# Kernel tuning notes

Measured on AMD Instinct MI355X. Metric: run time of the kernel, lower is better.

Reference implementation:

```python
import jax, jax.numpy as jnp
import numpy as np


def setup_inputs() -> dict:
    key = jax.random.key(0)
    k1, k2 = jax.random.split(key)
    x_in = jax.random.normal(k1, (8, 16384, 64), dtype=jnp.float32)
    codebook = jax.random.normal(k2, (512, 64), dtype=jnp.float32)
    return {"x_in": x_in, "codebook": codebook}


def reference(x_in, codebook):
    # Euclidean distances x_in [B,N,D] vs codebook [K,D] -> [B,N,K]
    x_sq = jnp.sum(x_in * x_in, axis=-1, keepdims=True)            # [B,N,1]
    e_sq = jnp.sum(codebook * codebook, axis=-1)                   # [K]
    cross = jnp.einsum('bnd,kd->bnk', x_in, codebook)              # [B,N,K]
    d2 = x_sq + e_sq[None, None, :] - 2.0 * cross
    distances = jnp.sqrt(jnp.maximum(d2, 0.0))
    # argmin with keepdim, as in extract_indices
    indices = jnp.argmin(distances, axis=2, keepdims=True)         # [B,N,1]
    # apply_codebook: embedding lookup -> [B,N,1,D]
    quantized = codebook[indices]
    return quantized
```

## Files before the change

### kernel.cpp

```cpp
#include <hip/hip_runtime.h>

#define D    64
#define K    512
#define QTOT (8 * 16384)
#define THR  0.001f

typedef __attribute__((ext_vector_type(8))) short short8;
typedef __attribute__((ext_vector_type(4))) short short4v;
typedef __attribute__((ext_vector_type(4))) float f32x4;

__device__ __forceinline__ unsigned short f2bf(float f) {
    unsigned u = __builtin_bit_cast(unsigned, f);
    u = u + 0x7FFFu + ((u >> 16) & 1u);
    return (unsigned short)(u >> 16);
}
__device__ __forceinline__ float bf2f(unsigned short h) {
    unsigned u = ((unsigned)h) << 16;
    return __builtin_bit_cast(float, u);
}

__global__ __launch_bounds__(512) void prep2b_kernel(const float* __restrict__ cb,
        float* __restrict__ esq, unsigned short* __restrict__ eh2,
        unsigned short* __restrict__ el2) {
    const int tid = threadIdx.x;
    const int b   = blockIdx.x;
    const float4* cbv4 = (const float4*)cb;
    for (int c = b * 512 + tid; c < (K * D) / 4; c += 4096) {
        float4 v = cbv4[c];
        float vv[4] = {v.x, v.y, v.z, v.w};
        short4v hi, lo;
        #pragma unroll
        for (int j = 0; j < 4; ++j) {
            unsigned short hb = f2bf(vv[j]);
            float hf = bf2f(hb);
            unsigned short lb = f2bf(vv[j] - hf);
            hi[j] = (short)f2bf(-2.0f * hf);
            lo[j] = (short)f2bf(-2.0f * bf2f(lb));
        }
        ((short4v*)eh2)[c] = hi;
        ((short4v*)el2)[c] = lo;
    }
    if (tid < 64) {
        const int row = b * 64 + tid;
        const float4* rp = (const float4*)(cb + (size_t)row * D);
        float s = 0.f;
        #pragma unroll
        for (int i = 0; i < 16; ++i) {
            float4 v = rp[i];
            s = fmaf(v.x, v.x, s); s = fmaf(v.y, v.y, s);
            s = fmaf(v.z, v.z, s); s = fmaf(v.w, v.w, s);
        }
        esq[row] = s;
    }
}

__global__ __launch_bounds__(1024) void vq_mfma12(
        const float* __restrict__ x, const float* __restrict__ cb,
        const float* __restrict__ g_esq, const unsigned short* __restrict__ eh2,
        const unsigned short* __restrict__ el2, float* __restrict__ out) {

    __shared__ unsigned short s_e[2][K * D];
    __shared__ float s_esq[K];

    const int tid  = threadIdx.x;
    const int lane = tid & 63;
    const int qrow = lane & 15;
    const int kg   = lane >> 4;
    const int kg4  = kg * 4;
    const int wv   = __builtin_amdgcn_readfirstlane(tid >> 6);
    const int qw   = blockIdx.x * 512 + wv * 32;

    for (int c = tid; c < (K * D) / 8; c += 1024) {
        short8 hv = ((const short8*)eh2)[c];
        short8 lv = ((const short8*)el2)[c];
        int byteoff = c * 16;
        int row     = byteoff >> 7;
        int addr    = byteoff ^ ((row & 7) << 4);
        *(short8*)((char*)s_e[0] + addr) = hv;
        *(short8*)((char*)s_e[1] + addr) = lv;
    }
    if (tid < K) s_esq[tid] = g_esq[tid];
    __syncthreads();

    short8 xh[2][2], xl[2][2];
    #pragma unroll
    for (int qt = 0; qt < 2; ++qt) {
        #pragma unroll
        for (int h = 0; h < 2; ++h) {
            const float* p = x + (size_t)(qw + qt * 16 + qrow) * D + h * 32 + kg * 8;
            float4 v0 = *(const float4*)p;
            float4 v1 = *(const float4*)(p + 4);
            float vv[8] = {v0.x, v0.y, v0.z, v0.w, v1.x, v1.y, v1.z, v1.w};
            short8 th, tl;
            #pragma unroll
            for (int j = 0; j < 8; ++j) {
                unsigned short hb = f2bf(vv[j]);
                th[j] = (short)hb;
                tl[j] = (short)f2bf(vv[j] - bf2f(hb));
            }
            xh[qt][h] = th;
            xl[qt][h] = tl;
        }
    }

    float m1[2], m2[2];
    int   i1[2];
    #pragma unroll
    for (int qt = 0; qt < 2; ++qt) { m1[qt] = 3.4e38f; m2[qt] = 3.4e38f; i1[qt] = 0; }

    const int swz = (qrow & 7) << 4;
    const int ob  = qrow * 128 + kg * 16;
    const char* ph = (const char*)s_e[0];
    const char* pl = (const char*)s_e[1];
    const int o0 = ob ^ swz;
    const int o1 = (ob + 64) ^ swz;
    const float* pq = s_esq + kg4;

    #pragma unroll
    for (int t = 0; t < 32; ++t) {
        short8 eh0 = *(const short8*)(ph + o0 + t * 2048);
        short8 eh1 = *(const short8*)(ph + o1 + t * 2048);
        short8 el0 = *(const short8*)(pl + o0 + t * 2048);
        short8 el1 = *(const short8*)(pl + o1 + t * 2048);
        f32x4 eqv  = *(const f32x4*)(pq + t * 16);

        __builtin_amdgcn_s_setprio(1);
        f32x4 a0 = eqv, a1 = eqv;
        a0 = __builtin_amdgcn_mfma_f32_16x16x32_bf16(eh0, xh[0][0], a0, 0, 0, 0);
        a1 = __builtin_amdgcn_mfma_f32_16x16x32_bf16(eh0, xh[1][0], a1, 0, 0, 0);
        a0 = __builtin_amdgcn_mfma_f32_16x16x32_bf16(eh1, xh[0][1], a0, 0, 0, 0);
        a1 = __builtin_amdgcn_mfma_f32_16x16x32_bf16(eh1, xh[1][1], a1, 0, 0, 0);
        a0 = __builtin_amdgcn_mfma_f32_16x16x32_bf16(eh0, xl[0][0], a0, 0, 0, 0);
        a1 = __builtin_amdgcn_mfma_f32_16x16x32_bf16(eh0, xl[1][0], a1, 0, 0, 0);
        a0 = __builtin_amdgcn_mfma_f32_16x16x32_bf16(eh1, xl[0][1], a0, 0, 0, 0);
        a1 = __builtin_amdgcn_mfma_f32_16x16x32_bf16(eh1, xl[1][1], a1, 0, 0, 0);
        a0 = __builtin_amdgcn_mfma_f32_16x16x32_bf16(el0, xh[0][0], a0, 0, 0, 0);
        a1 = __builtin_amdgcn_mfma_f32_16x16x32_bf16(el0, xh[1][0], a1, 0, 0, 0);
        a0 = __builtin_amdgcn_mfma_f32_16x16x32_bf16(el1, xh[0][1], a0, 0, 0, 0);
        a1 = __builtin_amdgcn_mfma_f32_16x16x32_bf16(el1, xh[1][1], a1, 0, 0, 0);
        __builtin_amdgcn_s_setprio(0);

        #pragma unroll
        for (int r = 0; r < 4; ++r) {
            float dd = a0[r];
            int   kc = (t * 16) | (kg4 + r);
            bool  lt = dd < m1[0];
            m2[0] = fminf(fmaxf(m1[0], dd), m2[0]);
            m1[0] = lt ? dd : m1[0];
            i1[0] = lt ? kc : i1[0];
        }
        #pragma unroll
        for (int r = 0; r < 4; ++r) {
            float dd = a1[r];
            int   kc = (t * 16) | (kg4 + r);
            bool  lt = dd < m1[1];
            m2[1] = fminf(fmaxf(m1[1], dd), m2[1]);
            m1[1] = lt ? dd : m1[1];
            i1[1] = lt ? kc : i1[1];
        }
    }

    #pragma unroll
    for (int qt = 0; qt < 2; ++qt) {
        #pragma unroll
        for (int off = 16; off <= 32; off <<= 1) {
            float om1 = __shfl_xor(m1[qt], off, 64);
            float om2 = __shfl_xor(m2[qt], off, 64);
            int   oi  = __shfl_xor(i1[qt], off, 64);
            bool  lt  = om1 < m1[qt];
            float loser = lt ? m1[qt] : om1;
            m2[qt] = fminf(fminf(m2[qt], om2), loser);
            m1[qt] = lt ? om1 : m1[qt];
            i1[qt] = lt ? oi  : i1[qt];
        }
    }

    #pragma unroll
    for (int qt = 0; qt < 2; ++qt) {
        bool flag = (m2[qt] - m1[qt]) <= THR;
        unsigned long long mask = __ballot(flag && (lane < 16));
        while (mask) {
            int ql = __ffsll(mask) - 1;
            mask &= mask - 1;
            int qf = qw + qt * 16 + ql;
            const float* xq = x + (size_t)qf * D;
            float bb = 3.4e38f;
            int   bq = 0;
            #pragma unroll 1
            for (int c0 = 0; c0 < 8; ++c0) {
                int kc = lane * 8 + c0;
                const float4* ep = (const float4*)(cb + (size_t)kc * D);
                float a = 0.f;
                #pragma unroll
                for (int i = 0; i < 16; ++i) {
                    float4 e = ep[i];
                    a = fmaf(xq[4 * i + 0], e.x, a);
                    a = fmaf(xq[4 * i + 1], e.y, a);
                    a = fmaf(xq[4 * i + 2], e.z, a);
                    a = fmaf(xq[4 * i + 3], e.w, a);
                }
                float dd = fmaf(-2.f, a, s_esq[kc]);
                if (dd < bb) { bb = dd; bq = kc; }
            }
            #pragma unroll
            for (int off = 1; off < 64; off <<= 1) {
                float ob = __shfl_xor(bb, off, 64);
                int   oq = __shfl_xor(bq, off, 64);
                if (ob < bb || (ob == bb && oq < bq)) { bb = ob; bq = oq; }
            }
            if (qrow == ql) i1[qt] = bq;
        }
    }

    #pragma unroll
    for (int qt = 0; qt < 2; ++qt) {
        size_t q = (size_t)(qw + qt * 16 + qrow);
        const float4* src = (const float4*)(cb + (size_t)i1[qt] * D) + kg * 4;
        float4*       dst = (float4*)(out + q * D) + kg * 4;
        #pragma unroll
        for (int s = 0; s < 4; ++s) dst[s] = src[s];
    }
}

__global__ __launch_bounds__(512) void vq_mfma(
        const float* __restrict__ x, const float* __restrict__ cb,
        float* __restrict__ out) {

    __shared__ unsigned short s_e[2][K * D];
    __shared__ float s_esq[K];

    const int tid  = threadIdx.x;
    const int lane = tid & 63;
    const int qrow = lane & 15;
    const int kg   = lane >> 4;
    const int wv   = __builtin_amdgcn_readfirstlane(tid >> 6);
    const int qw   = blockIdx.x * 512 + wv * 64;

    const float4* cbv4 = (const float4*)cb;
    for (int c = tid; c < (K * D) / 4; c += 512) {
        float4 v = cbv4[c];
        float vv[4] = {v.x, v.y, v.z, v.w};
        short4v hi, lo;
        #pragma unroll
        for (int j = 0; j < 4; ++j) {
            unsigned short hb = f2bf(vv[j]);
            hi[j] = (short)hb;
            lo[j] = (short)f2bf(vv[j] - bf2f(hb));
        }
        int byteoff = c * 8;
        int row     = byteoff >> 7;
        int addr    = byteoff ^ ((row & 7) << 4);
        *(short4v*)((char*)s_e[0] + addr) = hi;
        *(short4v*)((char*)s_e[1] + addr) = lo;
    }
    {
        float s = 0.f;
        #pragma unroll
        for (int d = 0; d < D; ++d) {
            float v = cb[tid * D + d];
            s = fmaf(v, v, s);
        }
        s_esq[tid] = s;
    }
    __syncthreads();

    short8 xh[4][2], xl[4][2];
    #pragma unroll
    for (int qt = 0; qt < 4; ++qt) {
        #pragma unroll
        for (int h = 0; h < 2; ++h) {
            const float* p = x + (size_t)(qw + qt * 16 + qrow) * D + h * 32 + kg * 8;
            float4 v0 = *(const float4*)p;
            float4 v1 = *(const float4*)(p + 4);
            float vv[8] = {v0.x, v0.y, v0.z, v0.w, v1.x, v1.y, v1.z, v1.w};
            short8 th, tl;
            #pragma unroll
            for (int j = 0; j < 8; ++j) {
                unsigned short hb = f2bf(vv[j]);
                th[j] = (short)hb;
                tl[j] = (short)f2bf(vv[j] - bf2f(hb));
            }
            xh[qt][h] = th;
            xl[qt][h] = tl;
        }
    }

    float m1[4], m2[4];
    int   i1[4];
    #pragma unroll
    for (int qt = 0; qt < 4; ++qt) { m1[qt] = 3.4e38f; m2[qt] = 3.4e38f; i1[qt] = 0; }

    const f32x4 zacc = {0.f, 0.f, 0.f, 0.f};

    for (int t = 0; t < 32; ++t) {
        const int row  = t * 16 + qrow;
        const int swz  = (row & 7) << 4;
        const int off0 = row * 128 + kg * 16;
        short8 eh0 = *(const short8*)((const char*)s_e[0] + ((off0     ) ^ swz));
        short8 eh1 = *(const short8*)((const char*)s_e[0] + ((off0 + 64) ^ swz));
        short8 el0 = *(const short8*)((const char*)s_e[1] + ((off0     ) ^ swz));
        short8 el1 = *(const short8*)((const char*)s_e[1] + ((off0 + 64) ^ swz));
        f32x4 eq = *(const f32x4*)(s_esq + t * 16 + kg * 4);

        #pragma unroll
        for (int qt = 0; qt < 4; ++qt) {
            f32x4 acc;
            asm volatile(
                "s_nop 3\n\t"
                "v_mfma_f32_16x16x32_bf16 %0, %1, %5, %9\n\t"
                "v_mfma_f32_16x16x32_bf16 %0, %2, %6, %0\n\t"
                "v_mfma_f32_16x16x32_bf16 %0, %1, %7, %0\n\t"
                "v_mfma_f32_16x16x32_bf16 %0, %2, %8, %0\n\t"
                "v_mfma_f32_16x16x32_bf16 %0, %3, %5, %0\n\t"
                "v_mfma_f32_16x16x32_bf16 %0, %4, %6, %0\n\t"
                "s_nop 7\n\t"
                "s_nop 7"
                : "=&v"(acc)
                : "v"(eh0), "v"(eh1), "v"(el0), "v"(el1),
                  "v"(xh[qt][0]), "v"(xh[qt][1]), "v"(xl[qt][0]), "v"(xl[qt][1]),
                  "v"(zacc));
            #pragma unroll
            for (int r = 0; r < 4; ++r) {
                float dd = fmaf(-2.f, acc[r], eq[r]);
                int   kc = t * 16 + kg * 4 + r;
                bool  lt = dd < m1[qt];
                m2[qt] = lt ? m1[qt] : fminf(m2[qt], dd);
                m1[qt] = lt ? dd : m1[qt];
                i1[qt] = lt ? kc : i1[qt];
            }
        }
    }

    #pragma unroll
    for (int qt = 0; qt < 4; ++qt) {
        #pragma unroll
        for (int off = 16; off <= 32; off <<= 1) {
            float om1 = __shfl_xor(m1[qt], off, 64);
            float om2 = __shfl_xor(m2[qt], off, 64);
            int   oi  = __shfl_xor(i1[qt], off, 64);
            bool  lt  = om1 < m1[qt];
            float loser = lt ? m1[qt] : om1;
            m2[qt] = fminf(fminf(m2[qt], om2), loser);
            m1[qt] = lt ? om1 : m1[qt];
            i1[qt] = lt ? oi  : i1[qt];
        }
    }

    #pragma unroll
    for (int qt = 0; qt < 4; ++qt) {
        bool flag = (m2[qt] - m1[qt]) <= 0.008f;
        unsigned long long mask = __ballot(flag && (lane < 16));
        while (mask) {
            int ql = __ffsll(mask) - 1;
            mask &= mask - 1;
            int qf = qw + qt * 16 + ql;
            const float* xq = x + (size_t)qf * D;
            float bb = 3.4e38f;
            int   bq = 0;
            #pragma unroll 1
            for (int c0 = 0; c0 < 8; ++c0) {
                int kc = lane * 8 + c0;
                const float4* ep = (const float4*)(cb + (size_t)kc * D);
                float a = 0.f;
                #pragma unroll
                for (int i = 0; i < 16; ++i) {
                    float4 e = ep[i];
                    a = fmaf(xq[4 * i + 0], e.x, a);
                    a = fmaf(xq[4 * i + 1], e.y, a);
                    a = fmaf(xq[4 * i + 2], e.z, a);
                    a = fmaf(xq[4 * i + 3], e.w, a);
                }
                float dd = fmaf(-2.f, a, s_esq[kc]);
                if (dd < bb) { bb = dd; bq = kc; }
            }
            #pragma unroll
            for (int off = 1; off < 64; off <<= 1) {
                float ob = __shfl_xor(bb, off, 64);
                int   oq = __shfl_xor(bq, off, 64);
                if (ob < bb || (ob == bb && oq < bq)) { bb = ob; bq = oq; }
            }
            if (qrow == ql) i1[qt] = bq;
        }
    }

    #pragma unroll
    for (int qt = 0; qt < 4; ++qt) {
        size_t q = (size_t)(qw + qt * 16 + qrow);
        const float4* src = (const float4*)(cb + (size_t)i1[qt] * D) + kg * 4;
        float4*       dst = (float4*)(out + q * D) + kg * 4;
        #pragma unroll
        for (int s = 0; s < 4; ++s) dst[s] = src[s];
    }
}

extern "C" void kernel_launch(void* const* d_in, const int* in_sizes, int n_in,
                              void* d_out, int out_size, void* d_ws, size_t ws_size,
                              hipStream_t stream) {
    const float* x   = (const float*)d_in[0];
    const float* cb  = (const float*)d_in[1];
    float*       out = (float*)d_out;

    const size_t need = 2048 + (size_t)K * D * 2 * 2;
    if (ws_size >= need) {
        float*          esq = (float*)d_ws;
        unsigned short* eh2 = (unsigned short*)((char*)d_ws + 2048);
        unsigned short* el2 = (unsigned short*)((char*)d_ws + 2048 + K * D * 2);
        prep2b_kernel<<<8, 512, 0, stream>>>(cb, esq, eh2, el2);
        vq_mfma12<<<QTOT / 512, 1024, 0, stream>>>(x, cb, esq, eh2, el2, out);
    } else {
        vq_mfma<<<QTOT / 512, 512, 0, stream>>>(x, cb, out);
    }
}
```

Before: 48.44 us.

## Split codebook across two blocks and merge partial argmins in a combine kernel

The main kernel now splits the codebook into two 256-entry halves, each handled by its own block, with one 16-query tile per wave. This halves shared memory per block and doubles the grid so more blocks can be resident. Each half writes a partial (min, second min, index) into the output buffer as scratch. A new combine kernel merges the two halves, reruns the exact fp32 fallback for near-ties, and gathers the codebook row. The cost is an extra launch, an extra pass over the output, and x being loaded by both halves.

Result: slower. 61.00 us (+25.9%).

```diff
diff --git a/kernel.cpp b/kernel.cpp
--- a/kernel.cpp
+++ b/kernel.cpp
@@ -2,6 +2,7 @@
 
 #define D    64
 #define K    512
+#define KH   256
 #define QTOT (8 * 16384)
 #define THR  0.001f
 
@@ -54,13 +55,13 @@
     }
 }
 
-__global__ __launch_bounds__(1024) void vq_mfma12(
-        const float* __restrict__ x, const float* __restrict__ cb,
-        const float* __restrict__ g_esq, const unsigned short* __restrict__ eh2,
-        const unsigned short* __restrict__ el2, float* __restrict__ out) {
-
-    __shared__ unsigned short s_e[2][K * D];
-    __shared__ float s_esq[K];
+__global__ __launch_bounds__(1024, 8) void vq_half(
+        const float* __restrict__ x, const float* __restrict__ g_esq,
+        const unsigned short* __restrict__ eh2, const unsigned short* __restrict__ el2,
+        float* __restrict__ out) {
+
+    __shared__ unsigned short s_e[2][KH * D];
+    __shared__ float s_esq[KH];
 
     const int tid  = threadIdx.x;
     const int lane = tid & 63;
@@ -68,45 +69,49 @@
     const int kg   = lane >> 4;
     const int kg4  = kg * 4;
     const int wv   = __builtin_amdgcn_readfirstlane(tid >> 6);
-    const int qw   = blockIdx.x * 512 + wv * 32;
-
-    for (int c = tid; c < (K * D) / 8; c += 1024) {
-        short8 hv = ((const short8*)eh2)[c];
-        short8 lv = ((const short8*)el2)[c];
-        int byteoff = c * 16;
-        int row     = byteoff >> 7;
-        int addr    = byteoff ^ ((row & 7) << 4);
-        *(short8*)((char*)s_e[0] + addr) = hv;
-        *(short8*)((char*)s_e[1] + addr) = lv;
-    }
-    if (tid < K) s_esq[tid] = g_esq[tid];
+    const int qb   = blockIdx.x & 511;
+    const int bh   = blockIdx.x >> 9;
+    const int kbase = bh * KH;
+    const int qw   = qb * 256 + wv * 16;
+
+    {
+        const short8* src_h = (const short8*)eh2 + (size_t)bh * (KH * D / 8);
+        const short8* src_l = (const short8*)el2 + (size_t)bh * (KH * D / 8);
+        #pragma unroll
+        for (int it = 0; it < 2; ++it) {
+            int c = tid + it * 1024;
+            short8 hv = src_h[c];
+            short8 lv = src_l[c];
+            int byteoff = c * 16;
+            int row     = byteoff >> 7;
+            int addr    = byteoff ^ ((row & 7) << 4);
+            *(short8*)((char*)s_e[0] + addr) = hv;
+            *(short8*)((char*)s_e[1] + addr) = lv;
+        }
+    }
+    if (tid < KH) s_esq[tid] = g_esq[kbase + tid];
     __syncthreads();
 
-    short8 xh[2][2], xl[2][2];
-    #pragma unroll
-    for (int qt = 0; qt < 2; ++qt) {
-        #pragma unroll
-        for (int h = 0; h < 2; ++h) {
-            const float* p = x + (size_t)(qw + qt * 16 + qrow) * D + h * 32 + kg * 8;
-            float4 v0 = *(const float4*)p;
-            float4 v1 = *(const float4*)(p + 4);
-            float vv[8] = {v0.x, v0.y, v0.z, v0.w, v1.x, v1.y, v1.z, v1.w};
-            short8 th, tl;
-            #pragma unroll
-            for (int j = 0; j < 8; ++j) {
-                unsigned short hb = f2bf(vv[j]);
-                th[j] = (short)hb;
-                tl[j] = (short)f2bf(vv[j] - bf2f(hb));
-            }
-            xh[qt][h] = th;
-            xl[qt][h] = tl;
-        }
-    }
-
-    float m1[2], m2[2];
-    int   i1[2];
-    #pragma unroll
-    for (int qt = 0; qt < 2; ++qt) { m1[qt] = 3.4e38f; m2[qt] = 3.4e38f; i1[qt] = 0; }
+    short8 xh[2], xl[2];
+    #pragma unroll
+    for (int h = 0; h < 2; ++h) {
+        const float* p = x + (size_t)(qw + qrow) * D + h * 32 + kg * 8;
+        float4 v0 = *(const float4*)p;
+        float4 v1 = *(const float4*)(p + 4);
+        float vv[8] = {v0.x, v0.y, v0.z, v0.w, v1.x, v1.y, v1.z, v1.w};
+        short8 th, tl;
+        #pragma unroll
+        for (int j = 0; j < 8; ++j) {
+            unsigned short hb = f2bf(vv[j]);
+            th[j] = (short)hb;
+            tl[j] = (short)f2bf(vv[j] - bf2f(hb));
+        }
+        xh[h] = th;
+        xl[h] = tl;
+    }
+
+    float m1 = 3.4e38f, m2 = 3.4e38f;
+    int   i1 = kbase;
 
     const int swz = (qrow & 7) << 4;
     const int ob  = qrow * 128 + kg * 16;
@@ -117,7 +122,7 @@
     const float* pq = s_esq + kg4;
 
     #pragma unroll
-    for (int t = 0; t < 32; ++t) {
+    for (int t = 0; t < 16; ++t) {
         short8 eh0 = *(const short8*)(ph + o0 + t * 2048);
         short8 eh1 = *(const short8*)(ph + o1 + t * 2048);
         short8 el0 = *(const short8*)(pl + o0 + t * 2048);
@@ -125,64 +130,77 @@
         f32x4 eqv  = *(const f32x4*)(pq + t * 16);
 
         __builtin_amdgcn_s_setprio(1);
-        f32x4 a0 = eqv, a1 = eqv;
-        a0 = __builtin_amdgcn_mfma_f32_16x16x32_bf16(eh0, xh[0][0], a0, 0, 0, 0);
-        a1 = __builtin_amdgcn_mfma_f32_16x16x32_bf16(eh0, xh[1][0], a1, 0, 0, 0);
-        a0 = __builtin_amdgcn_mfma_f32_16x16x32_bf16(eh1, xh[0][1], a0, 0, 0, 0);
-        a1 = __builtin_amdgcn_mfma_f32_16x16x32_bf16(eh1, xh[1][1], a1, 0, 0, 0);
-        a0 = __builtin_amdgcn_mfma_f32_16x16x32_bf16(eh0, xl[0][0], a0, 0, 0, 0);
-        a1 = __builtin_amdgcn_mfma_f32_16x16x32_bf16(eh0, xl[1][0], a1, 0, 0, 0);
-        a0 = __builtin_amdgcn_mfma_f32_16x16x32_bf16(eh1, xl[0][1], a0, 0, 0, 0);
-        a1 = __builtin_amdgcn_mfma_f32_16x16x32_bf16(eh1, xl[1][1], a1, 0, 0, 0);
-        a0 = __builtin_amdgcn_mfma_f32_16x16x32_bf16(el0, xh[0][0], a0, 0, 0, 0);
-        a1 = __builtin_amdgcn_mfma_f32_16x16x32_bf16(el0, xh[1][0], a1, 0, 0, 0);
-        a0 = __builtin_amdgcn_mfma_f32_16x16x32_bf16(el1, xh[0][1], a0, 0, 0, 0);
-        a1 = __builtin_amdgcn_mfma_f32_16x16x32_bf16(el1, xh[1][1], a1, 0, 0, 0);
+        f32x4 a0 = eqv;
+        a0 = __builtin_amdgcn_mfma_f32_16x16x32_bf16(eh0, xh[0], a0, 0, 0, 0);
+        a0 = __builtin_amdgcn_mfma_f32_16x16x32_bf16(eh1, xh[1], a0, 0, 0, 0);
+        a0 = __builtin_amdgcn_mfma_f32_16x16x32_bf16(eh0, xl[0], a0, 0, 0, 0);
+        a0 = __builtin_amdgcn_mfma_f32_16x16x32_bf16(eh1, xl[1], a0, 0, 0, 0);
+        a0 = __builtin_amdgcn_mfma_f32_16x16x32_bf16(el0, xh[0], a0, 0, 0, 0);
+        a0 = __builtin_amdgcn_mfma_f32_16x16x32_bf16(el1, xh[1], a0, 0, 0, 0);
         __builtin_amdgcn_s_setprio(0);
 
         #pragma unroll
         for (int r = 0; r < 4; ++r) {
             float dd = a0[r];
-            int   kc = (t * 16) | (kg4 + r);
-            bool  lt = dd < m1[0];
-            m2[0] = fminf(fmaxf(m1[0], dd), m2[0]);
-            m1[0] = lt ? dd : m1[0];
-            i1[0] = lt ? kc : i1[0];
-        }
-        #pragma unroll
-        for (int r = 0; r < 4; ++r) {
-            float dd = a1[r];
-            int   kc = (t * 16) | (kg4 + r);
-            bool  lt = dd < m1[1];
-            m2[1] = fminf(fmaxf(m1[1], dd), m2[1]);
-            m1[1] = lt ? dd : m1[1];
-            i1[1] = lt ? kc : i1[1];
-        }
-    }
-
-    #pragma unroll
-    for (int qt = 0; qt < 2; ++qt) {
-        #pragma unroll
-        for (int off = 16; off <= 32; off <<= 1) {
-            float om1 = __shfl_xor(m1[qt], off, 64);
-            float om2 = __shfl_xor(m2[qt], off, 64);
-            int   oi  = __shfl_xor(i1[qt], off, 64);
-            bool  lt  = om1 < m1[qt];
-            float loser = lt ? m1[qt] : om1;
-            m2[qt] = fminf(fminf(m2[qt], om2), loser);
-            m1[qt] = lt ? om1 : m1[qt];
-            i1[qt] = lt ? oi  : i1[qt];
-        }
-    }
-
-    #pragma unroll
-    for (int qt = 0; qt < 2; ++qt) {
-        bool flag = (m2[qt] - m1[qt]) <= THR;
+            int   kc = kbase | (t * 16) | (kg4 + r);
+            bool  lt = dd < m1;
+            m2 = fminf(fmaxf(m1, dd), m2);
+            m1 = fminf(m1, dd);
+            i1 = lt ? kc : i1;
+        }
+    }
+
+    #pragma unroll
+    for (int off = 16; off <= 32; off <<= 1) {
+        float om1 = __shfl_xor(m1, off, 64);
+        float om2 = __shfl_xor(m2, off, 64);
+        int   oi  = __shfl_xor(i1, off, 64);
+        bool  lt  = om1 < m1;
+        float loser = lt ? m1 : om1;
+        m2 = fminf(fminf(m2, om2), loser);
+        m1 = lt ? om1 : m1;
+        i1 = lt ? oi  : i1;
+    }
+
+    if (lane < 16) {
+        float* row = out + (size_t)(qw + lane) * D + bh * 3;
+        row[0] = m1;
+        row[1] = m2;
+        row[2] = __builtin_bit_cast(float, i1);
+    }
+}
+
+__global__ __launch_bounds__(256) void combine_emit(
+        const float* __restrict__ x, const float* __restrict__ cb,
+        const float* __restrict__ esq, float* __restrict__ out) {
+
+    const int tid  = threadIdx.x;
+    const int lane = tid & 63;
+    const int qrow = lane & 15;
+    const int kg   = lane >> 4;
+    const int wv   = __builtin_amdgcn_readfirstlane(tid >> 6);
+    const int qw   = blockIdx.x * 64 + wv * 16;
+    const size_t q = (size_t)(qw + qrow);
+
+    float* row = out + q * D;
+    float m1a = row[0], m2a = row[1];
+    int   ia  = __builtin_bit_cast(int, row[2]);
+    float m1b = row[3], m2b = row[4];
+    int   ib  = __builtin_bit_cast(int, row[5]);
+
+    bool  lt = m1b < m1a;
+    float m1 = lt ? m1b : m1a;
+    int   i1 = lt ? ib  : ia;
+    float loser = lt ? m1a : m1b;
+    float m2 = fminf(fminf(m2a, m2b), loser);
+
+    {
+        bool flag = (m2 - m1) <= THR;
         unsigned long long mask = __ballot(flag && (lane < 16));
         while (mask) {
             int ql = __ffsll(mask) - 1;
             mask &= mask - 1;
-            int qf = qw + qt * 16 + ql;
+            int qf = qw + ql;
             const float* xq = x + (size_t)qf * D;
             float bb = 3.4e38f;
             int   bq = 0;
@@ -199,7 +217,7 @@
                     a = fmaf(xq[4 * i + 2], e.z, a);
                     a = fmaf(xq[4 * i + 3], e.w, a);
                 }
-                float dd = fmaf(-2.f, a, s_esq[kc]);
+                float dd = fmaf(-2.f, a, esq[kc]);
                 if (dd < bb) { bb = dd; bq = kc; }
             }
             #pragma unroll
@@ -208,18 +226,14 @@
                 int   oq = __shfl_xor(bq, off, 64);
                 if (ob < bb || (ob == bb && oq < bq)) { bb = ob; bq = oq; }
             }
-            if (qrow == ql) i1[qt] = bq;
-        }
-    }
-
-    #pragma unroll
-    for (int qt = 0; qt < 2; ++qt) {
-        size_t q = (size_t)(qw + qt * 16 + qrow);
-        const float4* src = (const float4*)(cb + (size_t)i1[qt] * D) + kg * 4;
-        float4*       dst = (float4*)(out + q * D) + kg * 4;
-        #pragma unroll
-        for (int s = 0; s < 4; ++s) dst[s] = src[s];
-    }
+            if (qrow == ql) i1 = bq;
+        }
+    }
+
+    const float4* src = (const float4*)(cb + (size_t)i1 * D) + kg * 4;
+    float4*       dst = (float4*)row + kg * 4;
+    #pragma unroll
+    for (int s = 0; s < 4; ++s) dst[s] = src[s];
 }
 
 __global__ __launch_bounds__(512) void vq_mfma(
@@ -406,7 +420,8 @@
         unsigned short* eh2 = (unsigned short*)((char*)d_ws + 2048);
         unsigned short* el2 = (unsigned short*)((char*)d_ws + 2048 + K * D * 2);
         prep2b_kernel<<<8, 512, 0, stream>>>(cb, esq, eh2, el2);
-        vq_mfma12<<<QTOT / 512, 1024, 0, stream>>>(x, cb, esq, eh2, el2, out);
+        vq_half<<<1024, 1024, 0, stream>>>(x, esq, eh2, el2, out);
+        combine_emit<<<QTOT / 64, 256, 0, stream>>>(x, cb, esq, out);
     } else {
         vq_mfma<<<QTOT / 512, 512, 0, stream>>>(x, cb, out);
     }
```
